# Optimization experiments

Hardware: AMD Instinct MI355X
Metric: run time of the kernel (lower is better)

## Reference

```python
import jax, jax.numpy as jnp
import numpy as np

N_NODES = 100000
N_EDGES = 1600000
IN_F = 128
OUT_F = 64
BN_EPS = 1e-5


def setup_inputs() -> dict:
    key = jax.random.key(0)
    ks = jax.random.split(key, 6)
    feature = jax.random.normal(ks[0], (N_NODES, IN_F), dtype=jnp.float32)
    src = jax.random.randint(ks[1], (N_EDGES,), 0, N_NODES, dtype=jnp.int32)
    dst = jax.random.randint(ks[2], (N_EDGES,), 0, N_NODES, dtype=jnp.int32)
    W = jax.random.normal(ks[3], (IN_F, OUT_F), dtype=jnp.float32) * 0.05
    b = jnp.zeros((OUT_F,), dtype=jnp.float32)
    res_W = jax.random.normal(ks[4], (IN_F, OUT_F), dtype=jnp.float32) * 0.05
    res_b = jnp.zeros((OUT_F,), dtype=jnp.float32)
    gamma = jnp.ones((OUT_F,), dtype=jnp.float32)
    beta = jnp.zeros((OUT_F,), dtype=jnp.float32)
    return {"feature": feature, "src": src, "dst": dst, "W": W, "b": b,
            "res_W": res_W, "res_b": res_b, "gamma": gamma, "beta": beta,
            "idx": 0}


def _gcn_layer(feature, src, dst, W, b, res_W, res_b, gamma, beta):
    n = feature.shape[0]
    ones = jnp.ones_like(src, dtype=feature.dtype)
    # DGL norm='both': src-side uses out-degree, dst-side uses in-degree,
    # degrees clamped to min 1 (allow_zero_in_degree=True).
    out_deg = jax.ops.segment_sum(ones, src, num_segments=n)
    in_deg = jax.ops.segment_sum(ones, dst, num_segments=n)
    norm_src = jax.lax.rsqrt(jnp.maximum(out_deg, 1.0))  # [N]
    norm_dst = jax.lax.rsqrt(jnp.maximum(in_deg, 1.0))   # [N]

    # in_feats (128) > out_feats (64): DGL multiplies by W before aggregation.
    h = (feature * norm_src[:, None]) @ W                 # [N, OUT_F]
    agg = jax.ops.segment_sum(h[src], dst, num_segments=n)  # [N, OUT_F]
    conv = jax.nn.relu(agg * norm_dst[:, None] + b)

    # residual connection: activation(Linear(feature))
    res = jax.nn.relu(feature @ res_W + res_b)
    y = conv + res

    # BatchNorm1d (training mode, biased variance)
    mean = jnp.mean(y, axis=0)
    var = jnp.mean(jnp.square(y - mean), axis=0)
    y = (y - mean) * jax.lax.rsqrt(var + BN_EPS) * gamma + beta
    return y


def reference(feature, src, dst, W, b, res_W, res_b, gamma, beta, idx):
    # idx == 0 -> dropout branch is skipped (eval-deterministic reference)
    return _gcn_layer(feature, src, dst, W, b, res_W, res_b, gamma, beta)
```

## Files before the change

kernel.cpp:

```cpp
#include <hip/hip_runtime.h>
#include <hip/hip_fp16.h>

#define NCOL 64
#define KDIM 128
#define NB 512
#define CH 4096

typedef short bf16x8 __attribute__((ext_vector_type(8)));
typedef float f32x4 __attribute__((ext_vector_type(4)));
typedef float f32x2 __attribute__((ext_vector_type(2)));

__device__ __forceinline__ unsigned short f2bf(float f) {
    unsigned int u = __float_as_uint(f);
    return (unsigned short)((u + 0x7fffu + ((u >> 16) & 1u)) >> 16);
}

__global__ __launch_bounds__(512) void hist_kernel(const int* __restrict__ src,
                                                   const int* __restrict__ dst,
                                                   int* __restrict__ outcnt,
                                                   int* __restrict__ bcnt,
                                                   int* __restrict__ gh, int E) {
    __shared__ int lh[NB];
    int tid = threadIdx.x;
    int c = blockIdx.x;
    if (tid < NB) lh[tid] = 0;
    __syncthreads();
    int c0 = c * CH;
    int cnt = min(CH, E - c0);
    for (int i = tid; i < cnt; i += 512) {
        atomicAdd(&outcnt[src[c0 + i]], 1);
        atomicAdd(&lh[dst[c0 + i] >> 8], 1);
    }
    __syncthreads();
    if (tid < NB) {
        int v = lh[tid];
        gh[(size_t)c * NB + tid] = v;
        if (v) atomicAdd(&bcnt[tid], v);
    }
}

__global__ __launch_bounds__(256) void bucket_scan(const int* __restrict__ bcnt,
                                                   int* __restrict__ bbase,
                                                   int* __restrict__ row_start, int N, int E) {
    __shared__ int wsum[8];
    int tid = threadIdx.x, lane = tid & 63, wv = tid >> 6;
    int a = bcnt[tid], b = bcnt[tid + 256];
    int ia = a, ib = b;
#pragma unroll
    for (int off = 1; off < 64; off <<= 1) {
        int t = __shfl_up(ia, off); if (lane >= off) ia += t;
        int u = __shfl_up(ib, off); if (lane >= off) ib += u;
    }
    if (lane == 63) { wsum[wv] = ia; wsum[4 + wv] = ib; }
    __syncthreads();
    if (tid == 0) { int run = 0; for (int i = 0; i < 8; ++i) { int t = wsum[i]; wsum[i] = run; run += t; } }
    __syncthreads();
    bbase[tid] = wsum[wv] + ia - a;
    bbase[tid + 256] = wsum[4 + wv] + ib - b;
    if (tid == 0) row_start[N] = E;
}

__global__ __launch_bounds__(256) void chunk_scan(int* __restrict__ gh,
                                                  const int* __restrict__ bbase, int nchunks) {
    __shared__ int wsum[4];
    __shared__ int carry_s, tot_s;
    int k = blockIdx.x;
    int tid = threadIdx.x, lane = tid & 63, wv = tid >> 6;
    if (tid == 0) carry_s = bbase[k];
    __syncthreads();
    for (int t0 = 0; t0 < nchunks; t0 += 256) {
        int c = t0 + tid;
        int x = (c < nchunks) ? gh[(size_t)c * NB + k] : 0;
        int inc = x;
#pragma unroll
        for (int off = 1; off < 64; off <<= 1) {
            int t = __shfl_up(inc, off); if (lane >= off) inc += t;
        }
        if (lane == 63) wsum[wv] = inc;
        __syncthreads();
        if (tid == 0) {
            int run = 0;
            for (int i = 0; i < 4; ++i) { int t = wsum[i]; wsum[i] = run; run += t; }
            tot_s = run;
        }
        __syncthreads();
        int excl = carry_s + wsum[wv] + inc - x;
        if (c < nchunks) gh[(size_t)c * NB + k] = excl;
        __syncthreads();
        if (tid == 0) carry_s += tot_s;
        __syncthreads();
    }
}

__global__ __launch_bounds__(512) void scatter_pk(const int* __restrict__ src,
                                                  const int* __restrict__ dst,
                                                  const int* __restrict__ gh,
                                                  unsigned int* __restrict__ pk, int E) {
    __shared__ int lcur[NB];
    int tid = threadIdx.x;
    int c = blockIdx.x;
    if (tid < NB) lcur[tid] = gh[(size_t)c * NB + tid];
    __syncthreads();
    int c0 = c * CH;
    int cnt = min(CH, E - c0);
    for (int i = tid; i < cnt; i += 512) {
        int s = src[c0 + i], d = dst[c0 + i];
        int pos = atomicAdd(&lcur[d >> 8], 1);
        pk[pos] = ((unsigned)(d & 255) << 17) | (unsigned)s;
    }
}

__global__ __launch_bounds__(256) void fine_kernel(
    const unsigned int* __restrict__ pk, const int* __restrict__ bbase,
    int* __restrict__ row_start, int* __restrict__ ssrc, int E, int nbuck, int N) {
    __shared__ int hist[256];
    __shared__ int cur[256];
    __shared__ int wsum[4];
    int k = blockIdx.x;
    int tid = threadIdx.x, lane = tid & 63, wv = tid >> 6;
    int b0 = bbase[k];
    int b1 = (k + 1 < nbuck) ? bbase[k + 1] : E;

    hist[tid] = 0;
    __syncthreads();
    for (int i = b0 + tid; i < b1; i += 256)
        atomicAdd(&hist[pk[i] >> 17], 1);
    __syncthreads();

    int x = hist[tid], inc = x;
#pragma unroll
    for (int off = 1; off < 64; off <<= 1) {
        int t = __shfl_up(inc, off); if (lane >= off) inc += t;
    }
    if (lane == 63) wsum[wv] = inc;
    __syncthreads();
    if (tid == 0) { int run = 0; for (int i = 0; i < 4; ++i) { int t = wsum[i]; wsum[i] = run; run += t; } }
    __syncthreads();
    int excl = wsum[wv] + inc - x;

    int d = (k << 8) + tid;
    if (d < N) row_start[d] = b0 + excl;
    cur[tid] = b0 + excl;
    __syncthreads();

    for (int i = b0 + tid; i < b1; i += 256) {
        unsigned int p = pk[i];
        int pos = atomicAdd(&cur[p >> 17], 1);
        ssrc[pos] = (int)(p & 0x1FFFFu);
    }
}

__global__ __launch_bounds__(256) void matmul_mfma(
    const float* __restrict__ feat, const float* __restrict__ W,
    const float* __restrict__ RW, const float* __restrict__ res_b,
    const int* __restrict__ outcnt,
    unsigned int* __restrict__ hb8, float* __restrict__ y, int N) {
    __shared__ bf16x8 Bf[2048];
    int tid = threadIdx.x;
    for (int idx = tid; idx < 2048; idx += 256) {
        int mat = idx >> 10;
        int kc = (idx >> 8) & 3;
        int ct = (idx >> 6) & 3;
        int l = idx & 63;
        const float* Wp = mat ? RW : W;
        int kbase = kc * 32 + (l >> 4) * 8;
        int col = ct * 16 + (l & 15);
        bf16x8 t;
#pragma unroll
        for (int j = 0; j < 8; ++j)
            t[j] = (short)f2bf(Wp[(size_t)(kbase + j) * NCOL + col]);
        Bf[idx] = t;
    }
    __syncthreads();

    int lane = tid & 63;
    int wid = tid >> 6;
    int ntiles = (N + 15) >> 4;
    int tile = blockIdx.x * 4 + wid;
    if (tile >= ntiles) return;
    int c16 = lane & 15, kg = lane >> 4;

    float rbv[4];
#pragma unroll
    for (int ct = 0; ct < 4; ++ct) rbv[ct] = res_b[ct * 16 + c16];

    int tb = tile << 4;
    f32x4 acch[4], accr[4];
#pragma unroll
    for (int ct = 0; ct < 4; ++ct) {
        acch[ct] = (f32x4){0.f, 0.f, 0.f, 0.f};
        accr[ct] = (f32x4){0.f, 0.f, 0.f, 0.f};
    }

    int arow = tb + c16; if (arow >= N) arow = N - 1;
    const float* fp = feat + (size_t)arow * KDIM + kg * 8;
#pragma unroll
    for (int kc = 0; kc < 4; ++kc) {
        float4 a0 = *(const float4*)(fp + kc * 32);
        float4 a1 = *(const float4*)(fp + kc * 32 + 4);
        bf16x8 af;
        af[0] = (short)f2bf(a0.x); af[1] = (short)f2bf(a0.y);
        af[2] = (short)f2bf(a0.z); af[3] = (short)f2bf(a0.w);
        af[4] = (short)f2bf(a1.x); af[5] = (short)f2bf(a1.y);
        af[6] = (short)f2bf(a1.z); af[7] = (short)f2bf(a1.w);
#pragma unroll
        for (int ct = 0; ct < 4; ++ct) {
            acch[ct] = __builtin_amdgcn_mfma_f32_16x16x32_bf16(
                af, Bf[(kc * 4 + ct) * 64 + lane], acch[ct], 0, 0, 0);
            accr[ct] = __builtin_amdgcn_mfma_f32_16x16x32_bf16(
                af, Bf[1024 + (kc * 4 + ct) * 64 + lane], accr[ct], 0, 0, 0);
        }
    }

    float nrm[4];
#pragma unroll
    for (int r = 0; r < 4; ++r) {
        int rw = tb + kg * 4 + r; if (rw >= N) rw = N - 1;
        nrm[r] = rsqrtf(fmaxf((float)outcnt[rw], 1.0f));
    }
#pragma unroll
    for (int r = 0; r < 4; ++r) {
        int row = tb + kg * 4 + r;
        if (row < N) {
            unsigned int p = 0;
            p = (unsigned int)__builtin_amdgcn_cvt_pk_fp8_f32(
                    acch[0][r] * nrm[r], acch[1][r] * nrm[r], (int)p, false);
            p = (unsigned int)__builtin_amdgcn_cvt_pk_fp8_f32(
                    acch[2][r] * nrm[r], acch[3][r] * nrm[r], (int)p, true);
#pragma unroll
            for (int ct = 0; ct < 4; ++ct)
                y[(size_t)row * NCOL + ct * 16 + c16] = fmaxf(accr[ct][r] + rbv[ct], 0.0f);
            hb8[(size_t)row * 16 + c16] = p;
        }
    }
}

#define GATHER_ROW_STEP(eBase, eEnd, A0, A1, A2, A3)                                   \
    {                                                                                   \
        int e0 = (eBase) + e4, e1 = e0 + 4, e2 = e0 + 8, e3 = e0 + 12;                  \
        int i0 = (e0 < (eEnd)) ? ssrc[e0] : -1;                                         \
        int i1 = (e1 < (eEnd)) ? ssrc[e1] : -1;                                         \
        int i2 = (e2 < (eEnd)) ? ssrc[e2] : -1;                                         \
        int i3 = (e3 < (eEnd)) ? ssrc[e3] : -1;                                         \
        unsigned int v0 = (i0 >= 0) ? hb8[(size_t)i0 * 16 + dw] : 0u;                   \
        unsigned int v1 = (i1 >= 0) ? hb8[(size_t)i1 * 16 + dw] : 0u;                   \
        unsigned int v2 = (i2 >= 0) ? hb8[(size_t)i2 * 16 + dw] : 0u;                   \
        unsigned int v3 = (i3 >= 0) ? hb8[(size_t)i3 * 16 + dw] : 0u;                   \
        f32x2 l0 = __builtin_amdgcn_cvt_pk_f32_fp8((int)v0, false);                     \
        f32x2 h0 = __builtin_amdgcn_cvt_pk_f32_fp8((int)v0, true);                      \
        f32x2 l1 = __builtin_amdgcn_cvt_pk_f32_fp8((int)v1, false);                     \
        f32x2 h1 = __builtin_amdgcn_cvt_pk_f32_fp8((int)v1, true);                      \
        f32x2 l2 = __builtin_amdgcn_cvt_pk_f32_fp8((int)v2, false);                     \
        f32x2 h2 = __builtin_amdgcn_cvt_pk_f32_fp8((int)v2, true);                      \
        f32x2 l3 = __builtin_amdgcn_cvt_pk_f32_fp8((int)v3, false);                     \
        f32x2 h3 = __builtin_amdgcn_cvt_pk_f32_fp8((int)v3, true);                      \
        A0 += (l0[0] + l1[0]) + (l2[0] + l3[0]);                                        \
        A1 += (l0[1] + l1[1]) + (l2[1] + l3[1]);                                        \
        A2 += (h0[0] + h1[0]) + (h2[0] + h3[0]);                                        \
        A3 += (h0[1] + h1[1]) + (h2[1] + h3[1]);                                        \
    }

__global__ __launch_bounds__(256) void gather_kernel(
    const int* __restrict__ row_start, const int* __restrict__ ssrc,
    const unsigned int* __restrict__ hb8, const float* __restrict__ b,
    float* __restrict__ y, float* __restrict__ stats, int N) {
    int tid = threadIdx.x, lane = tid & 63, wid = tid >> 6;
    int e4 = lane >> 4, dw = lane & 15;
    int rowSel = e4 >> 1;
    int colLo = ((e4 & 1) << 5) + dw;
    int wave = blockIdx.x * 4 + wid;
    int nwaves = gridDim.x * 4;

    float bcLo = b[colLo], bcHi = b[colLo + 16];
    float bnLo = 0.f, bnHi = 0.f, bnsqLo = 0.f, bnsqHi = 0.f;

    for (int d0 = wave * 2; d0 < N; d0 += 2 * nwaves) {
        int d1 = d0 + 1;
        int a0 = row_start[d0], a1 = row_start[d0 + 1];
        int b0e = 0, b1e = 0;
        if (d1 < N) { b0e = a1; b1e = row_start[d1 + 1]; }

        float A0 = 0.f, A1 = 0.f, A2 = 0.f, A3 = 0.f;
        float B0 = 0.f, B1 = 0.f, B2 = 0.f, B3 = 0.f;
        int nit = max((a1 - a0 + 15) >> 4, (b1e - b0e + 15) >> 4);
        for (int it = 0; it < nit; ++it) {
            GATHER_ROW_STEP(a0 + it * 16, a1, A0, A1, A2, A3)
            GATHER_ROW_STEP(b0e + it * 16, b1e, B0, B1, B2, B3)
        }

#pragma unroll
        for (int off = 16; off <= 32; off <<= 1) {
            A0 += __shfl_xor(A0, off); A1 += __shfl_xor(A1, off);
            A2 += __shfl_xor(A2, off); A3 += __shfl_xor(A3, off);
            B0 += __shfl_xor(B0, off); B1 += __shfl_xor(B1, off);
            B2 += __shfl_xor(B2, off); B3 += __shfl_xor(B3, off);
        }

        int dd = d0 + rowSel;
        if (dd < N) {
            int deg = rowSel ? (b1e - b0e) : (a1 - a0);
            float nd = rsqrtf(fmaxf((float)deg, 1.0f));
            float vLo = rowSel ? ((e4 & 1) ? B2 : B0) : ((e4 & 1) ? A2 : A0);
            float vHi = rowSel ? ((e4 & 1) ? B3 : B1) : ((e4 & 1) ? A3 : A1);
            float* yp = &y[(size_t)dd * NCOL + colLo];
            float v0 = fmaxf(vLo * nd + bcLo, 0.f) + yp[0];
            float v1 = fmaxf(vHi * nd + bcHi, 0.f) + yp[16];
            yp[0] = v0;
            yp[16] = v1;
            bnLo += v0; bnsqLo += v0 * v0;
            bnHi += v1; bnsqHi += v1 * v1;
        }
    }

    bnLo += __shfl_xor(bnLo, 32); bnsqLo += __shfl_xor(bnsqLo, 32);
    bnHi += __shfl_xor(bnHi, 32); bnsqHi += __shfl_xor(bnsqHi, 32);

    __shared__ float bnred[4][128];
    if (lane < 32) {
        bnred[wid][colLo] = bnLo;
        bnred[wid][colLo + 16] = bnHi;
        bnred[wid][64 + colLo] = bnsqLo;
        bnred[wid][64 + colLo + 16] = bnsqHi;
    }
    __syncthreads();
    if (tid < 128) {
        float v = bnred[0][tid] + bnred[1][tid] + bnred[2][tid] + bnred[3][tid];
        unsafeAtomicAdd(&stats[tid], v);
    }
}

__global__ __launch_bounds__(256) void apply_kernel(float* __restrict__ y,
                                                    const float* __restrict__ stats,
                                                    const float* __restrict__ gamma,
                                                    const float* __restrict__ beta,
                                                    float invN, int total4) {
    __shared__ float sc[64], sh[64];
    int tid = threadIdx.x;
    if (tid < 64) {
        float mean = stats[tid] * invN;
        float var = stats[64 + tid] * invN - mean * mean;
        float s = gamma[tid] * rsqrtf(var + 1e-5f);
        sc[tid] = s;
        sh[tid] = beta[tid] - mean * s;
    }
    __syncthreads();
    int i = blockIdx.x * blockDim.x + tid;
    int stride = gridDim.x * blockDim.x;
    float4* y4 = (float4*)y;
    for (; i < total4; i += stride) {
        float4 v = y4[i];
        int cbase = (i & 15) << 2;
        float4 s = *(const float4*)&sc[cbase];
        float4 t = *(const float4*)&sh[cbase];
        v.x = v.x * s.x + t.x;
        v.y = v.y * s.y + t.y;
        v.z = v.z * s.z + t.z;
        v.w = v.w * s.w + t.w;
        y4[i] = v;
    }
}

extern "C" void kernel_launch(void* const* d_in, const int* in_sizes, int n_in,
                              void* d_out, int out_size, void* d_ws, size_t ws_size,
                              hipStream_t stream) {
    const float* feat  = (const float*)d_in[0];
    const int*   src   = (const int*)d_in[1];
    const int*   dst   = (const int*)d_in[2];
    const float* W     = (const float*)d_in[3];
    const float* b     = (const float*)d_in[4];
    const float* RW    = (const float*)d_in[5];
    const float* rb    = (const float*)d_in[6];
    const float* gamma = (const float*)d_in[7];
    const float* beta  = (const float*)d_in[8];

    int N = in_sizes[0] / KDIM;
    int E = in_sizes[1];
    float* out = (float*)d_out;
    int nbuck = (N + 255) >> 8;
    int nchunks = (E + CH - 1) / CH;

    char* wsb = (char*)d_ws;
    unsigned int* hb8 = (unsigned int*)wsb;                wsb += (size_t)N * 16 * 4;
    unsigned int* pk  = (unsigned int*)wsb;                wsb += (size_t)E * 4;
    int*   ssrc     = (int*)wsb;                           wsb += (size_t)E * 4;
    int*   row_start= (int*)wsb;                           wsb += (size_t)(N + 1) * 4;
    int*   outcnt   = (int*)wsb;                           wsb += (size_t)N * 4;
    float* stats    = (float*)wsb;                         wsb += 256 * 4;
    int*   bcnt     = (int*)wsb;                           wsb += NB * 4;
    int*   bbase    = (int*)wsb;                           wsb += NB * 4;
    int*   gh       = (int*)wsb;

    hipMemsetAsync(outcnt, 0, ((size_t)N + 256 + NB) * 4, stream);

    hist_kernel<<<nchunks, 512, 0, stream>>>(src, dst, outcnt, bcnt, gh, E);
    bucket_scan<<<1, 256, 0, stream>>>(bcnt, bbase, row_start, N, E);
    matmul_mfma<<<(((N + 15) >> 4) + 3) / 4, 256, 0, stream>>>(feat, W, RW, rb, outcnt, hb8, out, N);
    chunk_scan<<<NB, 256, 0, stream>>>(gh, bbase, nchunks);
    scatter_pk<<<nchunks, 512, 0, stream>>>(src, dst, gh, pk, E);
    fine_kernel<<<nbuck, 256, 0, stream>>>(pk, bbase, row_start, ssrc, E, nbuck, N);
    gather_kernel<<<2048, 256, 0, stream>>>(row_start, ssrc, hb8, b, out, stats, N);
    apply_kernel<<<2048, 256, 0, stream>>>(out, stats, gamma, beta, 1.0f / (float)N, (N * NCOL) / 4);
}
```

Before: 239.1 us.

## Split edge gather by source half to localize hb8 reads in cache

```diff
diff --git a/kernel.cpp b/kernel.cpp
--- a/kernel.cpp
+++ b/kernel.cpp
@@ -14,6 +14,8 @@
     unsigned int u = __float_as_uint(f);
     return (unsigned short)((u + 0x7fffu + ((u >> 16) & 1u)) >> 16);
 }
+__device__ __forceinline__ float bflo(unsigned int u) { return __uint_as_float(u << 16); }
+__device__ __forceinline__ float bfhi(unsigned int u) { return __uint_as_float(u & 0xffff0000u); }
 
 __global__ __launch_bounds__(512) void hist_kernel(const int* __restrict__ src,
                                                    const int* __restrict__ dst,
@@ -39,35 +41,32 @@
     }
 }
 
-__global__ __launch_bounds__(256) void bucket_scan(const int* __restrict__ bcnt,
-                                                   int* __restrict__ bbase,
-                                                   int* __restrict__ row_start, int N, int E) {
-    __shared__ int wsum[8];
-    int tid = threadIdx.x, lane = tid & 63, wv = tid >> 6;
-    int a = bcnt[tid], b = bcnt[tid + 256];
-    int ia = a, ib = b;
-#pragma unroll
-    for (int off = 1; off < 64; off <<= 1) {
-        int t = __shfl_up(ia, off); if (lane >= off) ia += t;
-        int u = __shfl_up(ib, off); if (lane >= off) ib += u;
-    }
-    if (lane == 63) { wsum[wv] = ia; wsum[4 + wv] = ib; }
-    __syncthreads();
-    if (tid == 0) { int run = 0; for (int i = 0; i < 8; ++i) { int t = wsum[i]; wsum[i] = run; run += t; } }
-    __syncthreads();
-    bbase[tid] = wsum[wv] + ia - a;
-    bbase[tid + 256] = wsum[4 + wv] + ib - b;
-    if (tid == 0) row_start[N] = E;
-}
-
 __global__ __launch_bounds__(256) void chunk_scan(int* __restrict__ gh,
-                                                  const int* __restrict__ bbase, int nchunks) {
+                                                  const int* __restrict__ bcnt,
+                                                  int* __restrict__ bbase,
+                                                  int* __restrict__ row_start,
+                                                  int nchunks, int N, int E) {
     __shared__ int wsum[4];
+    __shared__ int red[4];
     __shared__ int carry_s, tot_s;
     int k = blockIdx.x;
     int tid = threadIdx.x, lane = tid & 63, wv = tid >> 6;
-    if (tid == 0) carry_s = bbase[k];
-    __syncthreads();
+
+    int v = 0;
+    if (tid < k) v = bcnt[tid];
+    if (tid + 256 < k) v += bcnt[tid + 256];
+#pragma unroll
+    for (int off = 1; off < 64; off <<= 1) v += __shfl_xor(v, off);
+    if (lane == 0) red[wv] = v;
+    __syncthreads();
+    if (tid == 0) {
+        int base = red[0] + red[1] + red[2] + red[3];
+        carry_s = base;
+        bbase[k] = base;
+        if (k == 0) row_start[N] = E;
+    }
+    __syncthreads();
+
     for (int t0 = 0; t0 < nchunks; t0 += 256) {
         int c = t0 + tid;
         int x = (c < nchunks) ? gh[(size_t)c * NB + k] : 0;
@@ -112,22 +111,26 @@
 
 __global__ __launch_bounds__(256) void fine_kernel(
     const unsigned int* __restrict__ pk, const int* __restrict__ bbase,
-    int* __restrict__ row_start, int* __restrict__ ssrc, int E, int nbuck, int N) {
-    __shared__ int hist[256];
-    __shared__ int cur[256];
+    int* __restrict__ row_start, int* __restrict__ row_mid, int* __restrict__ ssrc,
+    int E, int nbuck, int N, unsigned int Nhalf) {
+    __shared__ int hist[512];
+    __shared__ int cur[512];
     __shared__ int wsum[4];
     int k = blockIdx.x;
     int tid = threadIdx.x, lane = tid & 63, wv = tid >> 6;
     int b0 = bbase[k];
     int b1 = (k + 1 < nbuck) ? bbase[k + 1] : E;
 
-    hist[tid] = 0;
-    __syncthreads();
-    for (int i = b0 + tid; i < b1; i += 256)
-        atomicAdd(&hist[pk[i] >> 17], 1);
-    __syncthreads();
-
-    int x = hist[tid], inc = x;
+    hist[tid] = 0; hist[tid + 256] = 0;
+    __syncthreads();
+    for (int i = b0 + tid; i < b1; i += 256) {
+        unsigned int p = pk[i];
+        atomicAdd(&hist[((p >> 17) << 1) | ((p & 0x1FFFFu) >= Nhalf)], 1);
+    }
+    __syncthreads();
+
+    int lo = hist[2 * tid], hi = hist[2 * tid + 1];
+    int x = lo + hi, inc = x;
 #pragma unroll
     for (int off = 1; off < 64; off <<= 1) {
         int t = __shfl_up(inc, off); if (lane >= off) inc += t;
@@ -138,14 +141,18 @@
     __syncthreads();
     int excl = wsum[wv] + inc - x;
 
+    int baseLo = b0 + excl;
+    int baseHi = baseLo + lo;
     int d = (k << 8) + tid;
-    if (d < N) row_start[d] = b0 + excl;
-    cur[tid] = b0 + excl;
+    if (d < N) { row_start[d] = baseLo; row_mid[d] = baseHi; }
+    cur[2 * tid] = baseLo;
+    cur[2 * tid + 1] = baseHi;
     __syncthreads();
 
     for (int i = b0 + tid; i < b1; i += 256) {
         unsigned int p = pk[i];
-        int pos = atomicAdd(&cur[p >> 17], 1);
+        int key = ((p >> 17) << 1) | ((p & 0x1FFFFu) >= Nhalf);
+        int pos = atomicAdd(&cur[key], 1);
         ssrc[pos] = (int)(p & 0x1FFFFu);
     }
 }
@@ -235,57 +242,43 @@
     }
 }
 
-#define GATHER_ROW_STEP(eBase, eEnd, A0, A1, A2, A3)                                   \
+#define GATHER_STEP8(eBase, eEnd, A0, A1, A2, A3)                                      \
     {                                                                                   \
-        int e0 = (eBase) + e4, e1 = e0 + 4, e2 = e0 + 8, e3 = e0 + 12;                  \
+        int e0 = (eBase) + e4, e1 = e0 + 4;                                             \
         int i0 = (e0 < (eEnd)) ? ssrc[e0] : -1;                                         \
         int i1 = (e1 < (eEnd)) ? ssrc[e1] : -1;                                         \
-        int i2 = (e2 < (eEnd)) ? ssrc[e2] : -1;                                         \
-        int i3 = (e3 < (eEnd)) ? ssrc[e3] : -1;                                         \
         unsigned int v0 = (i0 >= 0) ? hb8[(size_t)i0 * 16 + dw] : 0u;                   \
         unsigned int v1 = (i1 >= 0) ? hb8[(size_t)i1 * 16 + dw] : 0u;                   \
-        unsigned int v2 = (i2 >= 0) ? hb8[(size_t)i2 * 16 + dw] : 0u;                   \
-        unsigned int v3 = (i3 >= 0) ? hb8[(size_t)i3 * 16 + dw] : 0u;                   \
         f32x2 l0 = __builtin_amdgcn_cvt_pk_f32_fp8((int)v0, false);                     \
         f32x2 h0 = __builtin_amdgcn_cvt_pk_f32_fp8((int)v0, true);                      \
         f32x2 l1 = __builtin_amdgcn_cvt_pk_f32_fp8((int)v1, false);                     \
         f32x2 h1 = __builtin_amdgcn_cvt_pk_f32_fp8((int)v1, true);                      \
-        f32x2 l2 = __builtin_amdgcn_cvt_pk_f32_fp8((int)v2, false);                     \
-        f32x2 h2 = __builtin_amdgcn_cvt_pk_f32_fp8((int)v2, true);                      \
-        f32x2 l3 = __builtin_amdgcn_cvt_pk_f32_fp8((int)v3, false);                     \
-        f32x2 h3 = __builtin_amdgcn_cvt_pk_f32_fp8((int)v3, true);                      \
-        A0 += (l0[0] + l1[0]) + (l2[0] + l3[0]);                                        \
-        A1 += (l0[1] + l1[1]) + (l2[1] + l3[1]);                                        \
-        A2 += (h0[0] + h1[0]) + (h2[0] + h3[0]);                                        \
-        A3 += (h0[1] + h1[1]) + (h2[1] + h3[1]);                                        \
-    }
-
-__global__ __launch_bounds__(256) void gather_kernel(
-    const int* __restrict__ row_start, const int* __restrict__ ssrc,
-    const unsigned int* __restrict__ hb8, const float* __restrict__ b,
-    float* __restrict__ y, float* __restrict__ stats, int N) {
+        A0 += l0[0] + l1[0]; A1 += l0[1] + l1[1];                                       \
+        A2 += h0[0] + h1[0]; A3 += h0[1] + h1[1];                                       \
+    }
+
+__global__ __launch_bounds__(256) void gather_lo(
+    const int* __restrict__ row_start, const int* __restrict__ row_mid,
+    const int* __restrict__ ssrc, const unsigned int* __restrict__ hb8,
+    unsigned int* __restrict__ part, int N) {
     int tid = threadIdx.x, lane = tid & 63, wid = tid >> 6;
     int e4 = lane >> 4, dw = lane & 15;
-    int rowSel = e4 >> 1;
-    int colLo = ((e4 & 1) << 5) + dw;
+    int rowSel = e4 >> 1, ch = e4 & 1;
     int wave = blockIdx.x * 4 + wid;
     int nwaves = gridDim.x * 4;
 
-    float bcLo = b[colLo], bcHi = b[colLo + 16];
-    float bnLo = 0.f, bnHi = 0.f, bnsqLo = 0.f, bnsqHi = 0.f;
-
     for (int d0 = wave * 2; d0 < N; d0 += 2 * nwaves) {
         int d1 = d0 + 1;
-        int a0 = row_start[d0], a1 = row_start[d0 + 1];
+        int a0 = row_start[d0], a1 = row_mid[d0];
         int b0e = 0, b1e = 0;
-        if (d1 < N) { b0e = a1; b1e = row_start[d1 + 1]; }
+        if (d1 < N) { b0e = row_start[d1]; b1e = row_mid[d1]; }
 
         float A0 = 0.f, A1 = 0.f, A2 = 0.f, A3 = 0.f;
         float B0 = 0.f, B1 = 0.f, B2 = 0.f, B3 = 0.f;
-        int nit = max((a1 - a0 + 15) >> 4, (b1e - b0e + 15) >> 4);
+        int nit = max((a1 - a0 + 7) >> 3, (b1e - b0e + 7) >> 3);
         for (int it = 0; it < nit; ++it) {
-            GATHER_ROW_STEP(a0 + it * 16, a1, A0, A1, A2, A3)
-            GATHER_ROW_STEP(b0e + it * 16, b1e, B0, B1, B2, B3)
+            GATHER_STEP8(a0 + it * 8, a1, A0, A1, A2, A3)
+            GATHER_STEP8(b0e + it * 8, b1e, B0, B1, B2, B3)
         }
 
 #pragma unroll
@@ -298,10 +291,61 @@
 
         int dd = d0 + rowSel;
         if (dd < N) {
-            int deg = rowSel ? (b1e - b0e) : (a1 - a0);
+            float vLo = rowSel ? (ch ? B2 : B0) : (ch ? A2 : A0);
+            float vHi = rowSel ? (ch ? B3 : B1) : (ch ? A3 : A1);
+            part[(size_t)dd * 32 + ch * 16 + dw] =
+                ((unsigned)f2bf(vHi) << 16) | f2bf(vLo);
+        }
+    }
+}
+
+__global__ __launch_bounds__(256) void gather_hi(
+    const int* __restrict__ row_start, const int* __restrict__ row_mid,
+    const int* __restrict__ ssrc, const unsigned int* __restrict__ hb8,
+    const unsigned int* __restrict__ part, const float* __restrict__ b,
+    float* __restrict__ y, float* __restrict__ stats, int N) {
+    int tid = threadIdx.x, lane = tid & 63, wid = tid >> 6;
+    int e4 = lane >> 4, dw = lane & 15;
+    int rowSel = e4 >> 1, ch = e4 & 1;
+    int colLo = (ch << 5) + dw;
+    int wave = blockIdx.x * 4 + wid;
+    int nwaves = gridDim.x * 4;
+
+    float bcLo = b[colLo], bcHi = b[colLo + 16];
+    float bnLo = 0.f, bnHi = 0.f, bnsqLo = 0.f, bnsqHi = 0.f;
+
+    for (int d0 = wave * 2; d0 < N; d0 += 2 * nwaves) {
+        int d1 = d0 + 1;
+        int rsA = row_start[d0];
+        int a0 = row_mid[d0], a1 = row_start[d0 + 1];
+        int b0e = 0, b1e = 0;
+        if (d1 < N) { b0e = row_mid[d1]; b1e = row_start[d1 + 1]; }
+
+        float A0 = 0.f, A1 = 0.f, A2 = 0.f, A3 = 0.f;
+        float B0 = 0.f, B1 = 0.f, B2 = 0.f, B3 = 0.f;
+        int nit = max((a1 - a0 + 7) >> 3, (b1e - b0e + 7) >> 3);
+        for (int it = 0; it < nit; ++it) {
+            GATHER_STEP8(a0 + it * 8, a1, A0, A1, A2, A3)
+            GATHER_STEP8(b0e + it * 8, b1e, B0, B1, B2, B3)
+        }
+
+#pragma unroll
+        for (int off = 16; off <= 32; off <<= 1) {
+            A0 += __shfl_xor(A0, off); A1 += __shfl_xor(A1, off);
+            A2 += __shfl_xor(A2, off); A3 += __shfl_xor(A3, off);
+            B0 += __shfl_xor(B0, off); B1 += __shfl_xor(B1, off);
+            B2 += __shfl_xor(B2, off); B3 += __shfl_xor(B3, off);
+        }
+
+        int dd = d0 + rowSel;
+        if (dd < N) {
+            int deg = rowSel ? (b1e - row_start[d1]) : (a1 - rsA);
             float nd = rsqrtf(fmaxf((float)deg, 1.0f));
-            float vLo = rowSel ? ((e4 & 1) ? B2 : B0) : ((e4 & 1) ? A2 : A0);
-            float vHi = rowSel ? ((e4 & 1) ? B3 : B1) : ((e4 & 1) ? A3 : A1);
+            float vLo = rowSel ? (ch ? B2 : B0) : (ch ? A2 : A0);
+            float vHi = rowSel ? (ch ? B3 : B1) : (ch ? A3 : A1);
+            unsigned int pp = part[(size_t)dd * 32 + ch * 16 + dw];
+            vLo += bflo(pp);
+            vHi += bfhi(pp);
             float* yp = &y[(size_t)dd * NCOL + colLo];
             float v0 = fmaxf(vLo * nd + bcLo, 0.f) + yp[0];
             float v1 = fmaxf(vHi * nd + bcHi, 0.f) + yp[16];
@@ -384,20 +428,23 @@
     unsigned int* pk  = (unsigned int*)wsb;                wsb += (size_t)E * 4;
     int*   ssrc     = (int*)wsb;                           wsb += (size_t)E * 4;
     int*   row_start= (int*)wsb;                           wsb += (size_t)(N + 1) * 4;
+    int*   row_mid  = (int*)wsb;                           wsb += (size_t)N * 4;
     int*   outcnt   = (int*)wsb;                           wsb += (size_t)N * 4;
     float* stats    = (float*)wsb;                         wsb += 256 * 4;
     int*   bcnt     = (int*)wsb;                           wsb += NB * 4;
     int*   bbase    = (int*)wsb;                           wsb += NB * 4;
-    int*   gh       = (int*)wsb;
+    int*   gh       = (int*)wsb;                           wsb += (size_t)nchunks * NB * 4;
+    unsigned int* part = (unsigned int*)wsb;
 
     hipMemsetAsync(outcnt, 0, ((size_t)N + 256 + NB) * 4, stream);
 
     hist_kernel<<<nchunks, 512, 0, stream>>>(src, dst, outcnt, bcnt, gh, E);
-    bucket_scan<<<1, 256, 0, stream>>>(bcnt, bbase, row_start, N, E);
     matmul_mfma<<<(((N + 15) >> 4) + 3) / 4, 256, 0, stream>>>(feat, W, RW, rb, outcnt, hb8, out, N);
-    chunk_scan<<<NB, 256, 0, stream>>>(gh, bbase, nchunks);
+    chunk_scan<<<NB, 256, 0, stream>>>(gh, bcnt, bbase, row_start, nchunks, N, E);
     scatter_pk<<<nchunks, 512, 0, stream>>>(src, dst, gh, pk, E);
-    fine_kernel<<<nbuck, 256, 0, stream>>>(pk, bbase, row_start, ssrc, E, nbuck, N);
-    gather_kernel<<<2048, 256, 0, stream>>>(row_start, ssrc, hb8, b, out, stats, N);
+    fine_kernel<<<nbuck, 256, 0, stream>>>(pk, bbase, row_start, row_mid, ssrc, E, nbuck, N,
+                                           (unsigned int)(N / 2));
+    gather_lo<<<2048, 256, 0, stream>>>(row_start, row_mid, ssrc, hb8, part, N);
+    gather_hi<<<2048, 256, 0, stream>>>(row_start, row_mid, ssrc, hb8, part, b, out, stats, N);
     apply_kernel<<<2048, 256, 0, stream>>>(out, stats, gamma, beta, 1.0f / (float)N, (N * NCOL) / 4);
 }
```

Result: slower. 253.9 us (+6.2%).

## Fold bucket scan into chunk_scan and gather four rows per wave

Applied to the files above, without the earlier changes.

```diff
diff --git a/kernel.cpp b/kernel.cpp
--- a/kernel.cpp
+++ b/kernel.cpp
@@ -39,35 +39,32 @@
     }
 }
 
-__global__ __launch_bounds__(256) void bucket_scan(const int* __restrict__ bcnt,
-                                                   int* __restrict__ bbase,
-                                                   int* __restrict__ row_start, int N, int E) {
-    __shared__ int wsum[8];
-    int tid = threadIdx.x, lane = tid & 63, wv = tid >> 6;
-    int a = bcnt[tid], b = bcnt[tid + 256];
-    int ia = a, ib = b;
-#pragma unroll
-    for (int off = 1; off < 64; off <<= 1) {
-        int t = __shfl_up(ia, off); if (lane >= off) ia += t;
-        int u = __shfl_up(ib, off); if (lane >= off) ib += u;
-    }
-    if (lane == 63) { wsum[wv] = ia; wsum[4 + wv] = ib; }
-    __syncthreads();
-    if (tid == 0) { int run = 0; for (int i = 0; i < 8; ++i) { int t = wsum[i]; wsum[i] = run; run += t; } }
-    __syncthreads();
-    bbase[tid] = wsum[wv] + ia - a;
-    bbase[tid + 256] = wsum[4 + wv] + ib - b;
-    if (tid == 0) row_start[N] = E;
-}
-
 __global__ __launch_bounds__(256) void chunk_scan(int* __restrict__ gh,
-                                                  const int* __restrict__ bbase, int nchunks) {
+                                                  const int* __restrict__ bcnt,
+                                                  int* __restrict__ bbase,
+                                                  int* __restrict__ row_start,
+                                                  int nchunks, int N, int E) {
     __shared__ int wsum[4];
+    __shared__ int red[4];
     __shared__ int carry_s, tot_s;
     int k = blockIdx.x;
     int tid = threadIdx.x, lane = tid & 63, wv = tid >> 6;
-    if (tid == 0) carry_s = bbase[k];
-    __syncthreads();
+
+    int v = 0;
+    if (tid < k) v = bcnt[tid];
+    if (tid + 256 < k) v += bcnt[tid + 256];
+#pragma unroll
+    for (int off = 1; off < 64; off <<= 1) v += __shfl_xor(v, off);
+    if (lane == 0) red[wv] = v;
+    __syncthreads();
+    if (tid == 0) {
+        int base = red[0] + red[1] + red[2] + red[3];
+        carry_s = base;
+        bbase[k] = base;
+        if (k == 0) row_start[N] = E;
+    }
+    __syncthreads();
+
     for (int t0 = 0; t0 < nchunks; t0 += 256) {
         int c = t0 + tid;
         int x = (c < nchunks) ? gh[(size_t)c * NB + k] : 0;
@@ -235,92 +232,109 @@
     }
 }
 
-#define GATHER_ROW_STEP(eBase, eEnd, A0, A1, A2, A3)                                   \
-    {                                                                                   \
-        int e0 = (eBase) + e4, e1 = e0 + 4, e2 = e0 + 8, e3 = e0 + 12;                  \
-        int i0 = (e0 < (eEnd)) ? ssrc[e0] : -1;                                         \
-        int i1 = (e1 < (eEnd)) ? ssrc[e1] : -1;                                         \
-        int i2 = (e2 < (eEnd)) ? ssrc[e2] : -1;                                         \
-        int i3 = (e3 < (eEnd)) ? ssrc[e3] : -1;                                         \
-        unsigned int v0 = (i0 >= 0) ? hb8[(size_t)i0 * 16 + dw] : 0u;                   \
-        unsigned int v1 = (i1 >= 0) ? hb8[(size_t)i1 * 16 + dw] : 0u;                   \
-        unsigned int v2 = (i2 >= 0) ? hb8[(size_t)i2 * 16 + dw] : 0u;                   \
-        unsigned int v3 = (i3 >= 0) ? hb8[(size_t)i3 * 16 + dw] : 0u;                   \
-        f32x2 l0 = __builtin_amdgcn_cvt_pk_f32_fp8((int)v0, false);                     \
-        f32x2 h0 = __builtin_amdgcn_cvt_pk_f32_fp8((int)v0, true);                      \
-        f32x2 l1 = __builtin_amdgcn_cvt_pk_f32_fp8((int)v1, false);                     \
-        f32x2 h1 = __builtin_amdgcn_cvt_pk_f32_fp8((int)v1, true);                      \
-        f32x2 l2 = __builtin_amdgcn_cvt_pk_f32_fp8((int)v2, false);                     \
-        f32x2 h2 = __builtin_amdgcn_cvt_pk_f32_fp8((int)v2, true);                      \
-        f32x2 l3 = __builtin_amdgcn_cvt_pk_f32_fp8((int)v3, false);                     \
-        f32x2 h3 = __builtin_amdgcn_cvt_pk_f32_fp8((int)v3, true);                      \
-        A0 += (l0[0] + l1[0]) + (l2[0] + l3[0]);                                        \
-        A1 += (l0[1] + l1[1]) + (l2[1] + l3[1]);                                        \
-        A2 += (h0[0] + h1[0]) + (h2[0] + h3[0]);                                        \
-        A3 += (h0[1] + h1[1]) + (h2[1] + h3[1]);                                        \
-    }
-
 __global__ __launch_bounds__(256) void gather_kernel(
     const int* __restrict__ row_start, const int* __restrict__ ssrc,
     const unsigned int* __restrict__ hb8, const float* __restrict__ b,
     float* __restrict__ y, float* __restrict__ stats, int N) {
     int tid = threadIdx.x, lane = tid & 63, wid = tid >> 6;
     int e4 = lane >> 4, dw = lane & 15;
-    int rowSel = e4 >> 1;
-    int colLo = ((e4 & 1) << 5) + dw;
     int wave = blockIdx.x * 4 + wid;
     int nwaves = gridDim.x * 4;
 
-    float bcLo = b[colLo], bcHi = b[colLo + 16];
-    float bnLo = 0.f, bnHi = 0.f, bnsqLo = 0.f, bnsqHi = 0.f;
-
-    for (int d0 = wave * 2; d0 < N; d0 += 2 * nwaves) {
-        int d1 = d0 + 1;
-        int a0 = row_start[d0], a1 = row_start[d0 + 1];
-        int b0e = 0, b1e = 0;
-        if (d1 < N) { b0e = a1; b1e = row_start[d1 + 1]; }
-
-        float A0 = 0.f, A1 = 0.f, A2 = 0.f, A3 = 0.f;
-        float B0 = 0.f, B1 = 0.f, B2 = 0.f, B3 = 0.f;
-        int nit = max((a1 - a0 + 15) >> 4, (b1e - b0e + 15) >> 4);
-        for (int it = 0; it < nit; ++it) {
-            GATHER_ROW_STEP(a0 + it * 16, a1, A0, A1, A2, A3)
-            GATHER_ROW_STEP(b0e + it * 16, b1e, B0, B1, B2, B3)
-        }
-
-#pragma unroll
-        for (int off = 16; off <= 32; off <<= 1) {
-            A0 += __shfl_xor(A0, off); A1 += __shfl_xor(A1, off);
-            A2 += __shfl_xor(A2, off); A3 += __shfl_xor(A3, off);
-            B0 += __shfl_xor(B0, off); B1 += __shfl_xor(B1, off);
-            B2 += __shfl_xor(B2, off); B3 += __shfl_xor(B3, off);
-        }
-
-        int dd = d0 + rowSel;
+    float bc[4];
+#pragma unroll
+    for (int j = 0; j < 4; ++j) bc[j] = b[16 * j + dw];
+    float bn[4] = {0.f, 0.f, 0.f, 0.f};
+    float bq[4] = {0.f, 0.f, 0.f, 0.f};
+
+    for (int d0 = wave * 4; d0 < N; d0 += nwaves * 4) {
+        int s0[4], s1[4];
+#pragma unroll
+        for (int r = 0; r < 4; ++r) {
+            int d = d0 + r;
+            s0[r] = (d < N) ? row_start[d] : 0;
+            s1[r] = (d < N) ? row_start[d + 1] : 0;
+        }
+        int nitmax = 0;
+#pragma unroll
+        for (int r = 0; r < 4; ++r) nitmax = max(nitmax, (s1[r] - s0[r] + 15) >> 4);
+
+        float A[4][4];
+#pragma unroll
+        for (int r = 0; r < 4; ++r)
+#pragma unroll
+            for (int j = 0; j < 4; ++j) A[r][j] = 0.f;
+
+        for (int it = 0; it < nitmax; ++it) {
+            int idx[4][4];
+#pragma unroll
+            for (int r = 0; r < 4; ++r) {
+                int eb = s0[r] + it * 16 + e4;
+#pragma unroll
+                for (int u = 0; u < 4; ++u) {
+                    int e = eb + u * 4;
+                    idx[r][u] = (e < s1[r]) ? ssrc[e] : -1;
+                }
+            }
+            unsigned int v[4][4];
+#pragma unroll
+            for (int r = 0; r < 4; ++r)
+#pragma unroll
+                for (int u = 0; u < 4; ++u)
+                    v[r][u] = (idx[r][u] >= 0) ? hb8[(size_t)idx[r][u] * 16 + dw] : 0u;
+#pragma unroll
+            for (int r = 0; r < 4; ++r)
+#pragma unroll
+                for (int u = 0; u < 4; ++u) {
+                    f32x2 lo = __builtin_amdgcn_cvt_pk_f32_fp8((int)v[r][u], false);
+                    f32x2 hi = __builtin_amdgcn_cvt_pk_f32_fp8((int)v[r][u], true);
+                    A[r][0] += lo[0]; A[r][1] += lo[1];
+                    A[r][2] += hi[0]; A[r][3] += hi[1];
+                }
+        }
+
+#pragma unroll
+        for (int r = 0; r < 4; ++r)
+#pragma unroll
+            for (int j = 0; j < 4; ++j) {
+                A[r][j] += __shfl_xor(A[r][j], 16);
+                A[r][j] += __shfl_xor(A[r][j], 32);
+            }
+
+        int dd = d0 + e4;
         if (dd < N) {
-            int deg = rowSel ? (b1e - b0e) : (a1 - a0);
+            int deg = s1[0] - s0[0];
+            deg = (e4 == 1) ? (s1[1] - s0[1]) : deg;
+            deg = (e4 == 2) ? (s1[2] - s0[2]) : deg;
+            deg = (e4 == 3) ? (s1[3] - s0[3]) : deg;
             float nd = rsqrtf(fmaxf((float)deg, 1.0f));
-            float vLo = rowSel ? ((e4 & 1) ? B2 : B0) : ((e4 & 1) ? A2 : A0);
-            float vHi = rowSel ? ((e4 & 1) ? B3 : B1) : ((e4 & 1) ? A3 : A1);
-            float* yp = &y[(size_t)dd * NCOL + colLo];
-            float v0 = fmaxf(vLo * nd + bcLo, 0.f) + yp[0];
-            float v1 = fmaxf(vHi * nd + bcHi, 0.f) + yp[16];
-            yp[0] = v0;
-            yp[16] = v1;
-            bnLo += v0; bnsqLo += v0 * v0;
-            bnHi += v1; bnsqHi += v1 * v1;
-        }
-    }
-
-    bnLo += __shfl_xor(bnLo, 32); bnsqLo += __shfl_xor(bnsqLo, 32);
-    bnHi += __shfl_xor(bnHi, 32); bnsqHi += __shfl_xor(bnsqHi, 32);
-
+            float* yp = &y[(size_t)dd * NCOL + dw];
+#pragma unroll
+            for (int j = 0; j < 4; ++j) {
+                float vj = A[0][j];
+                vj = (e4 == 1) ? A[1][j] : vj;
+                vj = (e4 == 2) ? A[2][j] : vj;
+                vj = (e4 == 3) ? A[3][j] : vj;
+                float vv = fmaxf(vj * nd + bc[j], 0.f) + yp[16 * j];
+                yp[16 * j] = vv;
+                bn[j] += vv;
+                bq[j] += vv * vv;
+            }
+        }
+    }
+
+#pragma unroll
+    for (int j = 0; j < 4; ++j) {
+        bn[j] += __shfl_xor(bn[j], 16); bn[j] += __shfl_xor(bn[j], 32);
+        bq[j] += __shfl_xor(bq[j], 16); bq[j] += __shfl_xor(bq[j], 32);
+    }
     __shared__ float bnred[4][128];
-    if (lane < 32) {
-        bnred[wid][colLo] = bnLo;
-        bnred[wid][colLo + 16] = bnHi;
-        bnred[wid][64 + colLo] = bnsqLo;
-        bnred[wid][64 + colLo + 16] = bnsqHi;
+    if (lane < 16) {
+#pragma unroll
+        for (int j = 0; j < 4; ++j) {
+            bnred[wid][16 * j + lane] = bn[j];
+            bnred[wid][64 + 16 * j + lane] = bq[j];
+        }
     }
     __syncthreads();
     if (tid < 128) {
@@ -393,9 +407,8 @@
     hipMemsetAsync(outcnt, 0, ((size_t)N + 256 + NB) * 4, stream);
 
     hist_kernel<<<nchunks, 512, 0, stream>>>(src, dst, outcnt, bcnt, gh, E);
-    bucket_scan<<<1, 256, 0, stream>>>(bcnt, bbase, row_start, N, E);
     matmul_mfma<<<(((N + 15) >> 4) + 3) / 4, 256, 0, stream>>>(feat, W, RW, rb, outcnt, hb8, out, N);
-    chunk_scan<<<NB, 256, 0, stream>>>(gh, bbase, nchunks);
+    chunk_scan<<<NB, 256, 0, stream>>>(gh, bcnt, bbase, row_start, nchunks, N, E);
     scatter_pk<<<nchunks, 512, 0, stream>>>(src, dst, gh, pk, E);
     fine_kernel<<<nbuck, 256, 0, stream>>>(pk, bbase, row_start, ssrc, E, nbuck, N);
     gather_kernel<<<2048, 256, 0, stream>>>(row_start, ssrc, hb8, b, out, stats, N);
```

Result: no change. 237.0 us (-0.9%).

## Fuse bucket scan into chunk scan, move out-degree count, store residual as bf16

Applied to the files above, without the earlier changes.

```diff
diff --git a/kernel.cpp b/kernel.cpp
--- a/kernel.cpp
+++ b/kernel.cpp
@@ -4,7 +4,7 @@
 #define NCOL 64
 #define KDIM 128
 #define NB 512
-#define CH 4096
+#define CH 8192
 
 typedef short bf16x8 __attribute__((ext_vector_type(8)));
 typedef float f32x4 __attribute__((ext_vector_type(4)));
@@ -14,10 +14,10 @@
     unsigned int u = __float_as_uint(f);
     return (unsigned short)((u + 0x7fffu + ((u >> 16) & 1u)) >> 16);
 }
-
-__global__ __launch_bounds__(512) void hist_kernel(const int* __restrict__ src,
-                                                   const int* __restrict__ dst,
-                                                   int* __restrict__ outcnt,
+__device__ __forceinline__ float bflo(unsigned int u) { return __uint_as_float(u << 16); }
+__device__ __forceinline__ float bfhi(unsigned int u) { return __uint_as_float(u & 0xffff0000u); }
+
+__global__ __launch_bounds__(512) void hist_kernel(const int* __restrict__ dst,
                                                    int* __restrict__ bcnt,
                                                    int* __restrict__ gh, int E) {
     __shared__ int lh[NB];
@@ -27,10 +27,8 @@
     __syncthreads();
     int c0 = c * CH;
     int cnt = min(CH, E - c0);
-    for (int i = tid; i < cnt; i += 512) {
-        atomicAdd(&outcnt[src[c0 + i]], 1);
+    for (int i = tid; i < cnt; i += 512)
         atomicAdd(&lh[dst[c0 + i] >> 8], 1);
-    }
     __syncthreads();
     if (tid < NB) {
         int v = lh[tid];
@@ -39,35 +37,32 @@
     }
 }
 
-__global__ __launch_bounds__(256) void bucket_scan(const int* __restrict__ bcnt,
-                                                   int* __restrict__ bbase,
-                                                   int* __restrict__ row_start, int N, int E) {
-    __shared__ int wsum[8];
-    int tid = threadIdx.x, lane = tid & 63, wv = tid >> 6;
-    int a = bcnt[tid], b = bcnt[tid + 256];
-    int ia = a, ib = b;
-#pragma unroll
-    for (int off = 1; off < 64; off <<= 1) {
-        int t = __shfl_up(ia, off); if (lane >= off) ia += t;
-        int u = __shfl_up(ib, off); if (lane >= off) ib += u;
-    }
-    if (lane == 63) { wsum[wv] = ia; wsum[4 + wv] = ib; }
-    __syncthreads();
-    if (tid == 0) { int run = 0; for (int i = 0; i < 8; ++i) { int t = wsum[i]; wsum[i] = run; run += t; } }
-    __syncthreads();
-    bbase[tid] = wsum[wv] + ia - a;
-    bbase[tid + 256] = wsum[4 + wv] + ib - b;
-    if (tid == 0) row_start[N] = E;
-}
-
 __global__ __launch_bounds__(256) void chunk_scan(int* __restrict__ gh,
-                                                  const int* __restrict__ bbase, int nchunks) {
+                                                  const int* __restrict__ bcnt,
+                                                  int* __restrict__ bbase,
+                                                  int* __restrict__ row_start,
+                                                  int nchunks, int N, int E) {
     __shared__ int wsum[4];
+    __shared__ int red[4];
     __shared__ int carry_s, tot_s;
     int k = blockIdx.x;
     int tid = threadIdx.x, lane = tid & 63, wv = tid >> 6;
-    if (tid == 0) carry_s = bbase[k];
-    __syncthreads();
+
+    int v = 0;
+    if (tid < k) v = bcnt[tid];
+    if (tid + 256 < k) v += bcnt[tid + 256];
+#pragma unroll
+    for (int off = 1; off < 64; off <<= 1) v += __shfl_xor(v, off);
+    if (lane == 0) red[wv] = v;
+    __syncthreads();
+    if (tid == 0) {
+        int base = red[0] + red[1] + red[2] + red[3];
+        carry_s = base;
+        bbase[k] = base;
+        if (k == 0) row_start[N] = E;
+    }
+    __syncthreads();
+
     for (int t0 = 0; t0 < nchunks; t0 += 256) {
         int c = t0 + tid;
         int x = (c < nchunks) ? gh[(size_t)c * NB + k] : 0;
@@ -95,7 +90,8 @@
 __global__ __launch_bounds__(512) void scatter_pk(const int* __restrict__ src,
                                                   const int* __restrict__ dst,
                                                   const int* __restrict__ gh,
-                                                  unsigned int* __restrict__ pk, int E) {
+                                                  unsigned int* __restrict__ pk,
+                                                  int* __restrict__ outcnt, int E) {
     __shared__ int lcur[NB];
     int tid = threadIdx.x;
     int c = blockIdx.x;
@@ -105,6 +101,7 @@
     int cnt = min(CH, E - c0);
     for (int i = tid; i < cnt; i += 512) {
         int s = src[c0 + i], d = dst[c0 + i];
+        atomicAdd(&outcnt[s], 1);
         int pos = atomicAdd(&lcur[d >> 8], 1);
         pk[pos] = ((unsigned)(d & 255) << 17) | (unsigned)s;
     }
@@ -154,7 +151,7 @@
     const float* __restrict__ feat, const float* __restrict__ W,
     const float* __restrict__ RW, const float* __restrict__ res_b,
     const int* __restrict__ outcnt,
-    unsigned int* __restrict__ hb8, float* __restrict__ y, int N) {
+    unsigned int* __restrict__ hb8, unsigned int* __restrict__ r8, int N) {
     __shared__ bf16x8 Bf[2048];
     int tid = threadIdx.x;
     for (int idx = tid; idx < 2048; idx += 256) {
@@ -227,10 +224,13 @@
                     acch[0][r] * nrm[r], acch[1][r] * nrm[r], (int)p, false);
             p = (unsigned int)__builtin_amdgcn_cvt_pk_fp8_f32(
                     acch[2][r] * nrm[r], acch[3][r] * nrm[r], (int)p, true);
-#pragma unroll
-            for (int ct = 0; ct < 4; ++ct)
-                y[(size_t)row * NCOL + ct * 16 + c16] = fmaxf(accr[ct][r] + rbv[ct], 0.0f);
             hb8[(size_t)row * 16 + c16] = p;
+            float q0 = fmaxf(accr[0][r] + rbv[0], 0.0f);
+            float q1 = fmaxf(accr[1][r] + rbv[1], 0.0f);
+            float q2 = fmaxf(accr[2][r] + rbv[2], 0.0f);
+            float q3 = fmaxf(accr[3][r] + rbv[3], 0.0f);
+            r8[(size_t)row * 32 + c16]      = ((unsigned)f2bf(q1) << 16) | f2bf(q0);
+            r8[(size_t)row * 32 + 16 + c16] = ((unsigned)f2bf(q3) << 16) | f2bf(q2);
         }
     }
 }
@@ -262,12 +262,13 @@
 
 __global__ __launch_bounds__(256) void gather_kernel(
     const int* __restrict__ row_start, const int* __restrict__ ssrc,
-    const unsigned int* __restrict__ hb8, const float* __restrict__ b,
+    const unsigned int* __restrict__ hb8, const unsigned int* __restrict__ r8,
+    const float* __restrict__ b,
     float* __restrict__ y, float* __restrict__ stats, int N) {
     int tid = threadIdx.x, lane = tid & 63, wid = tid >> 6;
     int e4 = lane >> 4, dw = lane & 15;
-    int rowSel = e4 >> 1;
-    int colLo = ((e4 & 1) << 5) + dw;
+    int rowSel = e4 >> 1, ch = e4 & 1;
+    int colLo = (ch << 5) + dw;
     int wave = blockIdx.x * 4 + wid;
     int nwaves = gridDim.x * 4;
 
@@ -300,11 +301,12 @@
         if (dd < N) {
             int deg = rowSel ? (b1e - b0e) : (a1 - a0);
             float nd = rsqrtf(fmaxf((float)deg, 1.0f));
-            float vLo = rowSel ? ((e4 & 1) ? B2 : B0) : ((e4 & 1) ? A2 : A0);
-            float vHi = rowSel ? ((e4 & 1) ? B3 : B1) : ((e4 & 1) ? A3 : A1);
+            float vLo = rowSel ? (ch ? B2 : B0) : (ch ? A2 : A0);
+            float vHi = rowSel ? (ch ? B3 : B1) : (ch ? A3 : A1);
+            unsigned int rr = r8[(size_t)dd * 32 + ch * 16 + dw];
+            float v0 = fmaxf(vLo * nd + bcLo, 0.f) + bflo(rr);
+            float v1 = fmaxf(vHi * nd + bcHi, 0.f) + bfhi(rr);
             float* yp = &y[(size_t)dd * NCOL + colLo];
-            float v0 = fmaxf(vLo * nd + bcLo, 0.f) + yp[0];
-            float v1 = fmaxf(vHi * nd + bcHi, 0.f) + yp[16];
             yp[0] = v0;
             yp[16] = v1;
             bnLo += v0; bnsqLo += v0 * v0;
@@ -381,6 +383,7 @@
 
     char* wsb = (char*)d_ws;
     unsigned int* hb8 = (unsigned int*)wsb;                wsb += (size_t)N * 16 * 4;
+    unsigned int* r8  = (unsigned int*)wsb;                wsb += (size_t)N * 32 * 4;
     unsigned int* pk  = (unsigned int*)wsb;                wsb += (size_t)E * 4;
     int*   ssrc     = (int*)wsb;                           wsb += (size_t)E * 4;
     int*   row_start= (int*)wsb;                           wsb += (size_t)(N + 1) * 4;
@@ -392,12 +395,11 @@
 
     hipMemsetAsync(outcnt, 0, ((size_t)N + 256 + NB) * 4, stream);
 
-    hist_kernel<<<nchunks, 512, 0, stream>>>(src, dst, outcnt, bcnt, gh, E);
-    bucket_scan<<<1, 256, 0, stream>>>(bcnt, bbase, row_start, N, E);
-    matmul_mfma<<<(((N + 15) >> 4) + 3) / 4, 256, 0, stream>>>(feat, W, RW, rb, outcnt, hb8, out, N);
-    chunk_scan<<<NB, 256, 0, stream>>>(gh, bbase, nchunks);
-    scatter_pk<<<nchunks, 512, 0, stream>>>(src, dst, gh, pk, E);
+    hist_kernel<<<nchunks, 512, 0, stream>>>(dst, bcnt, gh, E);
+    chunk_scan<<<NB, 256, 0, stream>>>(gh, bcnt, bbase, row_start, nchunks, N, E);
+    scatter_pk<<<nchunks, 512, 0, stream>>>(src, dst, gh, pk, outcnt, E);
+    matmul_mfma<<<(((N + 15) >> 4) + 3) / 4, 256, 0, stream>>>(feat, W, RW, rb, outcnt, hb8, r8, N);
     fine_kernel<<<nbuck, 256, 0, stream>>>(pk, bbase, row_start, ssrc, E, nbuck, N);
-    gather_kernel<<<2048, 256, 0, stream>>>(row_start, ssrc, hb8, b, out, stats, N);
+    gather_kernel<<<2048, 256, 0, stream>>>(row_start, ssrc, hb8, r8, b, out, stats, N);
     apply_kernel<<<2048, 256, 0, stream>>>(out, stats, gamma, beta, 1.0f / (float)N, (N * NCOL) / 4);
 }
```

Measured after the change: 228.5 us (median of 2 runs). 1.05x faster.
